# Kernel optimization log

Hardware: AMD Instinct MI355X
Metric: run time of the kernel (lower is better)

Reference implementation:

```python
import jax, jax.numpy as jnp
import numpy as np

WINDOW = 11      # window_size init kwarg
SIGMA = 1.5      # hardcoded in kornia ssim
MAX_VAL = 1.0
EPS = 1e-12
C1 = (0.01 * MAX_VAL) ** 2
C2 = (0.03 * MAX_VAL) ** 2


def _gauss1d():
    # matches kornia get_gaussian_kernel1d for odd window
    x = jnp.arange(WINDOW, dtype=jnp.float32) - WINDOW // 2
    g = jnp.exp(-(x ** 2) / (2.0 * SIGMA ** 2))
    return g / jnp.sum(g)


def _gfilter(x, g):
    # separable depthwise gaussian filter with reflect padding (kornia filter2d default)
    B, C, H, W = x.shape
    p = WINDOW // 2
    xp = jnp.pad(x, ((0, 0), (0, 0), (p, p), (p, p)), mode='reflect')
    kv = jnp.broadcast_to(g.reshape(1, 1, WINDOW, 1), (C, 1, WINDOW, 1))
    kh = jnp.broadcast_to(g.reshape(1, 1, 1, WINDOW), (C, 1, 1, WINDOW))
    dn = ('NCHW', 'OIHW', 'NCHW')
    y = jax.lax.conv_general_dilated(xp, kv, (1, 1), 'VALID',
                                     dimension_numbers=dn, feature_group_count=C)
    y = jax.lax.conv_general_dilated(y, kh, (1, 1), 'VALID',
                                     dimension_numbers=dn, feature_group_count=C)
    return y


def setup_inputs() -> dict:
    key = jax.random.key(0)
    k1, k2 = jax.random.split(key)
    shape = (16, 3, 512, 512)
    img1 = jax.random.uniform(k1, shape, dtype=jnp.float32)
    img2 = jax.random.uniform(k2, shape, dtype=jnp.float32)
    return {"img1": img1, "img2": img2}


def reference(img1, img2):
    g = _gauss1d()
    mu1 = _gfilter(img1, g)
    mu2 = _gfilter(img2, g)
    mu1_sq = mu1 ** 2
    mu2_sq = mu2 ** 2
    mu1_mu2 = mu1 * mu2
    sigma1_sq = _gfilter(img1 ** 2, g) - mu1_sq
    sigma2_sq = _gfilter(img2 ** 2, g) - mu2_sq
    sigma12 = _gfilter(img1 * img2, g) - mu1_mu2
    num = (2.0 * mu1_mu2 + C1) * (2.0 * sigma12 + C2)
    den = (mu1_sq + mu2_sq + C1) * (sigma1_sq + sigma2_sq + C2)
    return num / (den + EPS)
```

## Files before the change

### kernel.cpp

```cpp
#include <hip/hip_runtime.h>
#include <stdint.h>

#define IW 512
#define IH 512
#define NPLANES 48
#define TX 128
#define TY 16
#define INR (TY + 10)
#define BUFW 144
#define SLOTS 8

typedef float f32x2 __attribute__((ext_vector_type(2)));

typedef __attribute__((address_space(1))) const uint32_t guint_t;
typedef __attribute__((address_space(3))) uint32_t luint_t;

#define WAITVM_(n) asm volatile("s_waitcnt vmcnt(" #n ")" ::: "memory")
#define WAITVM(n) WAITVM_(n)

static __device__ __forceinline__ f32x2 pk_mul(f32x2 a, f32x2 b) {
    f32x2 d; asm("v_pk_mul_f32 %0, %1, %2" : "=v"(d) : "v"(a), "v"(b)); return d;
}
static __device__ __forceinline__ f32x2 pk_fma_s(f32x2 a, f32x2 w, f32x2 c) {
    f32x2 d; asm("v_pk_fma_f32 %0, %1, %2, %3" : "=v"(d) : "v"(a), "s"(w), "v"(c)); return d;
}
static __device__ __forceinline__ f32x2 pk_mul_bh(f32x2 a, f32x2 w) {
    f32x2 d; asm("v_pk_mul_f32 %0, %1, %2 op_sel:[1,0] op_sel_hi:[1,1]"
                 : "=v"(d) : "v"(a), "s"(w)); return d;
}
static __device__ __forceinline__ f32x2 pk_fma_bh(f32x2 a, f32x2 w, f32x2 c) {
    f32x2 d; asm("v_pk_fma_f32 %0, %1, %2, %3 op_sel:[1,0,0] op_sel_hi:[1,1,1]"
                 : "=v"(d) : "v"(a), "s"(w), "v"(c)); return d;
}
static __device__ __forceinline__ f32x2 pk_fma_bl(f32x2 a, f32x2 w, f32x2 c) {
    f32x2 d; asm("v_pk_fma_f32 %0, %1, %2, %3 op_sel:[0,0,0] op_sel_hi:[0,1,1]"
                 : "=v"(d) : "v"(a), "s"(w), "v"(c)); return d;
}
static __device__ __forceinline__ float rcp_fast(float x) {
    float d; asm("v_rcp_f32 %0, %1" : "=v"(d) : "v"(x)); return d;
}

__device__ __forceinline__ int refl(int c) {
    c = (c < 0) ? -c : c;
    return (c > IW - 1) ? (2 * (IW - 1) - c) : c;
}

#define W0 0.00102838f
#define W1 0.00759873f
#define W2 0.03600078f
#define W3 0.10936070f
#define W4 0.21300555f
#define W5 0.26601174f
#define W6 0.21300555f
#define W7 0.10936070f
#define W8 0.03600078f
#define W9 0.00759873f
#define W10 0.00102838f

#define SSIM_BODY(JJ, HR, ISSUE_D, WAITN)                                       \
  {                                                                             \
    const int hr = (HR);                                                        \
    const int rs = hr & 7;                                                      \
    if (ISSUE_D) {                                                              \
        const int rr = refl(ty + hr);                  \
        const int ws = (hr + 5) & 7;                                            \
        if (dmaok) {                                                            \
            __builtin_amdgcn_global_load_lds((guint_t*)(p1 + (size_t)rr * IW + gcol), \
                                             (luint_t*)&buf[ws][0][0], 16, 0, 0);     \
            __builtin_amdgcn_global_load_lds((guint_t*)(p2 + (size_t)rr * IW + gcol), \
                                             (luint_t*)&buf[ws][1][0], 16, 0, 0);     \
        }                                                                       \
    }                                                                           \
    WAITVM(WAITN);                                                              \
     \
    f32x2 a1[7], a2[7];                                                         \
    {                                                                           \
        const f32x2* bp1 = (const f32x2*)&buf[rs][0][2 * l + 2];                \
        const f32x2* bp2 = (const f32x2*)&buf[rs][1][2 * l + 2];                \
        _Pragma("unroll")                                                       \
        for (int i = 0; i < 7; ++i) { a1[i] = bp1[i]; a2[i] = bp2[i]; }         \
    }                                                                           \
                                  \
    if (tx == 0) {                                                              \
        _Pragma("unroll")                                                       \
        for (int i = 1; i <= 5; ++i) {                                          \
            const int j = 2 * l + 2 + i;                                        \
            if (j < 8) {                                                        \
                const float v1 = buf[rs][0][16 - j];                            \
                const float v2 = buf[rs][1][16 - j];                            \
                if (i & 1) { a1[i >> 1].y = v1; a2[i >> 1].y = v2; }            \
                else       { a1[i >> 1].x = v1; a2[i >> 1].x = v2; }            \
            }                                                                   \
        }                                                                       \
    } else if (tx == IW - TX) {                                                 \
        _Pragma("unroll")                                                       \
        for (int i = 8; i <= 12; ++i) {                                         \
            const int j = 2 * l + 2 + i;                                        \
            if (j >= 136) {                                                     \
                const float v1 = buf[rs][0][270 - j];                           \
                const float v2 = buf[rs][1][270 - j];                           \
                if (i & 1) { a1[i >> 1].y = v1; a2[i >> 1].y = v2; }            \
                else       { a1[i >> 1].x = v1; a2[i >> 1].x = v2; }            \
            }                                                                   \
        }                                                                       \
    }                                                                           \
                               \
    f32x2 H0, H1, H2, H3, H4;                                                   \
    {                              \
        const f32x2 Q11 = pk_mul(a1[0], a1[0]);                                 \
        const f32x2 Q22 = pk_mul(a2[0], a2[0]);                                 \
        const f32x2 Q12 = pk_mul(a1[0], a2[0]);                                 \
        H0 = pk_mul_bh(a1[0], WH[0]);                                           \
        H1 = pk_mul_bh(a2[0], WH[0]);                                           \
        H2 = pk_mul_bh(Q11,  WH[0]);                                            \
        H3 = pk_mul_bh(Q22,  WH[0]);                                            \
        H4 = pk_mul_bh(Q12,  WH[0]);                                            \
    }                                                                           \
    _Pragma("unroll")                                                           \
    for (int i = 1; i <= 5; ++i) {                                              \
        const f32x2 Q11 = pk_mul(a1[i], a1[i]);                                 \
        const f32x2 Q22 = pk_mul(a2[i], a2[i]);                                 \
        const f32x2 Q12 = pk_mul(a1[i], a2[i]);                                 \
        H0 = pk_fma_bl(a1[i], WL[i], H0); H0 = pk_fma_bh(a1[i], WH[i], H0);     \
        H1 = pk_fma_bl(a2[i], WL[i], H1); H1 = pk_fma_bh(a2[i], WH[i], H1);     \
        H2 = pk_fma_bl(Q11,  WL[i], H2); H2 = pk_fma_bh(Q11,  WH[i], H2);       \
        H3 = pk_fma_bl(Q22,  WL[i], H3); H3 = pk_fma_bh(Q22,  WH[i], H3);       \
        H4 = pk_fma_bl(Q12,  WL[i], H4); H4 = pk_fma_bh(Q12,  WH[i], H4);       \
    }                                                                           \
    {                             \
        const f32x2 Q11 = pk_mul(a1[6], a1[6]);                                 \
        const f32x2 Q22 = pk_mul(a2[6], a2[6]);                                 \
        const f32x2 Q12 = pk_mul(a1[6], a2[6]);                                 \
        H0 = pk_fma_bl(a1[6], WL[6], H0);                                       \
        H1 = pk_fma_bl(a2[6], WL[6], H1);                                       \
        H2 = pk_fma_bl(Q11,  WL[6], H2);                                        \
        H3 = pk_fma_bl(Q22,  WL[6], H3);                                        \
        H4 = pk_fma_bl(Q12,  WL[6], H4);                                        \
    }                                                                           \
                                             \
    _Pragma("unroll")                                                           \
    for (int k = 0; k < 11; ++k) {                                              \
        const int o = hr - k;                                      \
        if (o >= 0 && o < TY) {                                                 \
            const int s = (((JJ) - k) % 11 + 11) % 11;        \
            const f32x2 w2 = {gw[k], gw[k]};                                    \
            acc[s][0] = pk_fma_s(H0, w2, acc[s][0]);                            \
            acc[s][1] = pk_fma_s(H1, w2, acc[s][1]);                            \
            acc[s][2] = pk_fma_s(H2, w2, acc[s][2]);                            \
            acc[s][3] = pk_fma_s(H3, w2, acc[s][3]);                            \
            acc[s][4] = pk_fma_s(H4, w2, acc[s][4]);                            \
        }                                                                       \
    }                                                                           \
                          \
    if (hr >= 10) {                                                             \
        const int o = hr - 10;                                                  \
        const int sc = ((JJ) + 1) % 11;                       \
        const f32x2 mu1 = acc[sc][0], mu2 = acc[sc][1];                         \
        const f32x2 m11 = acc[sc][2], m22 = acc[sc][3], m12 = acc[sc][4];       \
        const f32x2 mu1s = mu1 * mu1, mu2s = mu2 * mu2, mu12 = mu1 * mu2;       \
        const f32x2 s1 = m11 - mu1s, s2 = m22 - mu2s, s12 = m12 - mu12;         \
        const f32x2 num = (2.f * mu12 + 1e-4f) * (2.f * s12 + 9e-4f);           \
        f32x2 den = (mu1s + mu2s + 1e-4f) * (s1 + s2 + 9e-4f);                  \
        den = den + 1e-12f;                                                     \
        f32x2 rd; rd.x = rcp_fast(den.x); rd.y = rcp_fast(den.y);               \
        const f32x2 res = num * rd;                                             \
        _Pragma("unroll")                                                       \
        for (int a = 0; a < 5; ++a) { acc[sc][a].x = 0.f; acc[sc][a].y = 0.f; } \
        *(f32x2*)&po[(size_t)(ty + o) * IW + tx + 2 * l] = res;                 \
    }                                                                           \
  }

__launch_bounds__(64, 3)
__global__ void ssim_kernel(const float* __restrict__ img1,
                            const float* __restrict__ img2,
                            float* __restrict__ out)
{
    __shared__ float buf[SLOTS][2][BUFW];

    const int l  = threadIdx.x;
    const int tx = blockIdx.x * TX;
    const int ty = blockIdx.y * TY;
    const size_t pb = (size_t)blockIdx.z * (size_t)(IW * IH);
    const float* p1 = img1 + pb;
    const float* p2 = img2 + pb;
    float* po = out + pb;

    const float gw[11] = {W0,W1,W2,W3,W4,W5,W6,W7,W8,W9,W10};
    const f32x2 WH[6] = { {W0, 0.f}, {W2, W1}, {W4, W3}, {W6, W5}, {W8, W7}, {W10, W9} };
    const f32x2 WL[7] = { {0.f,0.f}, {W1, W0}, {W3, W2}, {W5, W4}, {W7, W6}, {W9, W8}, {0.f, W10} };

    const int gcol = tx - 8 + 4 * l;
    const bool dmaok = (l < 36) && (gcol >= 0) && (gcol < IW);

    #pragma unroll
    for (int pr = 0; pr < 5; ++pr) {
        const int r = refl(ty - 5 + pr);
        if (dmaok) {
            __builtin_amdgcn_global_load_lds((guint_t*)(p1 + (size_t)r * IW + gcol),
                                             (luint_t*)&buf[pr][0][0], 16, 0, 0);
            __builtin_amdgcn_global_load_lds((guint_t*)(p2 + (size_t)r * IW + gcol),
                                             (luint_t*)&buf[pr][1][0], 16, 0, 0);
        }
    }

    f32x2 acc[11][5];
    #pragma unroll
    for (int s = 0; s < 11; ++s) {
        #pragma unroll
        for (int a = 0; a < 5; ++a) { acc[s][a].x = 0.f; acc[s][a].y = 0.f; }
    }

    for (int hrb = 0; hrb < 22; hrb += 11) {
        #pragma unroll
        for (int jj = 0; jj < 11; ++jj) {
            SSIM_BODY(jj, hrb + jj, true, 10)
        }
    }
    SSIM_BODY(0, 22, false, 8)
    SSIM_BODY(1, 23, false, 6)
    SSIM_BODY(2, 24, false, 4)
    SSIM_BODY(3, 25, false, 2)
    WAITVM(0);
}

extern "C" void kernel_launch(void* const* d_in, const int* in_sizes, int n_in,
                              void* d_out, int out_size, void* d_ws, size_t ws_size,
                              hipStream_t stream) {
    const float* img1 = (const float*)d_in[0];
    const float* img2 = (const float*)d_in[1];
    float* out = (float*)d_out;
    dim3 grid(IW / TX, IH / TY, NPLANES);
    ssim_kernel<<<grid, dim3(64), 0, stream>>>(img1, img2, out);
}
```

Before: 81.31 us.

## Double tile height and software-pipeline row loads with horizontal compute

Doubles the rows per block from 16 to 32, so the 10-row vertical halo is amortized over more output rows. The loop is restructured so the LDS window read for the next row is issued after the current row's horizontal pass, overlapping load latency with compute. Launch bounds drop from 3 to 2 waves per unit to allow more registers for the held-ahead window. The trade is fewer blocks, lower occupancy and a deeper wait schedule that must stay correct against the 8-slot LDS ring.

After: 88.61 us. +9.0%, slower.

```diff
diff --git a/kernel.cpp b/kernel.cpp
--- a/kernel.cpp
+++ b/kernel.cpp
@@ -5,7 +5,7 @@
 #define IH 512
 #define NPLANES 48
 #define TX 128
-#define TY 16
+#define TY 32
 #define INR (TY + 10)
 #define BUFW 144
 #define SLOTS 8
@@ -57,54 +57,53 @@
 #define W9 0.00759873f
 #define W10 0.00102838f
 
-#define SSIM_BODY(JJ, HR, ISSUE_D, WAITN)                                       \
-  {                                                                             \
-    const int hr = (HR);                                                        \
-    const int rs = hr & 7;                                                      \
-    if (ISSUE_D) {                                                              \
-        const int rr = refl(ty + hr);                  \
-        const int ws = (hr + 5) & 7;                                            \
+#define ISSUE_ROW(HR5)                                                          \
+    {                                                                           \
+        const int rr = refl(ty - 5 + (HR5));                                    \
+        const int ws = (HR5) & 7;                                               \
         if (dmaok) {                                                            \
             __builtin_amdgcn_global_load_lds((guint_t*)(p1 + (size_t)rr * IW + gcol), \
                                              (luint_t*)&buf[ws][0][0], 16, 0, 0);     \
             __builtin_amdgcn_global_load_lds((guint_t*)(p2 + (size_t)rr * IW + gcol), \
                                              (luint_t*)&buf[ws][1][0], 16, 0, 0);     \
         }                                                                       \
-    }                                                                           \
-    WAITVM(WAITN);                                                              \
-     \
-    f32x2 a1[7], a2[7];                                                         \
+    }
+
+#define READ_WINDOW(RS)                                                         \
     {                                                                           \
-        const f32x2* bp1 = (const f32x2*)&buf[rs][0][2 * l + 2];                \
-        const f32x2* bp2 = (const f32x2*)&buf[rs][1][2 * l + 2];                \
+        const f32x2* bp1 = (const f32x2*)&buf[RS][0][2 * l + 2];                \
+        const f32x2* bp2 = (const f32x2*)&buf[RS][1][2 * l + 2];                \
         _Pragma("unroll")                                                       \
         for (int i = 0; i < 7; ++i) { a1[i] = bp1[i]; a2[i] = bp2[i]; }         \
-    }                                                                           \
-                                  \
-    if (tx == 0) {                                                              \
-        _Pragma("unroll")                                                       \
-        for (int i = 1; i <= 5; ++i) {                                          \
-            const int j = 2 * l + 2 + i;                                        \
-            if (j < 8) {                                                        \
-                const float v1 = buf[rs][0][16 - j];                            \
-                const float v2 = buf[rs][1][16 - j];                            \
-                if (i & 1) { a1[i >> 1].y = v1; a2[i >> 1].y = v2; }            \
-                else       { a1[i >> 1].x = v1; a2[i >> 1].x = v2; }            \
+        if (tx == 0) {                                                          \
+            _Pragma("unroll")                                                   \
+            for (int i = 1; i <= 5; ++i) {                                      \
+                const int j = 2 * l + 2 + i;                                    \
+                if (j < 8) {                                                    \
+                    const float v1 = buf[RS][0][16 - j];                        \
+                    const float v2 = buf[RS][1][16 - j];                        \
+                    if (i & 1) { a1[i >> 1].y = v1; a2[i >> 1].y = v2; }        \
+                    else       { a1[i >> 1].x = v1; a2[i >> 1].x = v2; }        \
+                }                                                               \
+            }                                                                   \
+        } else if (tx == IW - TX) {                                             \
+            _Pragma("unroll")                                                   \
+            for (int i = 8; i <= 12; ++i) {                                     \
+                const int j = 2 * l + 2 + i;                                    \
+                if (j >= 136) {                                                 \
+                    const float v1 = buf[RS][0][270 - j];                       \
+                    const float v2 = buf[RS][1][270 - j];                       \
+                    if (i & 1) { a1[i >> 1].y = v1; a2[i >> 1].y = v2; }        \
+                    else       { a1[i >> 1].x = v1; a2[i >> 1].x = v2; }        \
+                }                                                               \
             }                                                                   \
         }                                                                       \
-    } else if (tx == IW - TX) {                                                 \
-        _Pragma("unroll")                                                       \
-        for (int i = 8; i <= 12; ++i) {                                         \
-            const int j = 2 * l + 2 + i;                                        \
-            if (j >= 136) {                                                     \
-                const float v1 = buf[rs][0][270 - j];                           \
-                const float v2 = buf[rs][1][270 - j];                           \
-                if (i & 1) { a1[i >> 1].y = v1; a2[i >> 1].y = v2; }            \
-                else       { a1[i >> 1].x = v1; a2[i >> 1].x = v2; }            \
-            }                                                                   \
-        }                                                                       \
-    }                                                                           \
-                               \
+    }
+
+#define SSIM_STEP(JJ, HR, DO_ISSUE, WAITN, DO_READ)                             \
+  {                                                                             \
+    const int hr = (HR);                                                        \
+     \
     f32x2 H0, H1, H2, H3, H4;                                                   \
     {                              \
         const f32x2 Q11 = pk_mul(a1[0], a1[0]);                                 \
@@ -137,7 +136,13 @@
         H3 = pk_fma_bl(Q22,  WL[6], H3);                                        \
         H4 = pk_fma_bl(Q12,  WL[6], H4);                                        \
     }                                                                           \
-                                             \
+                   \
+    if (DO_ISSUE) ISSUE_ROW(hr + 5);                                            \
+    if (DO_READ) {                                                              \
+        WAITVM(WAITN);                                                          \
+        READ_WINDOW((hr + 1) & 7);                                              \
+    }                                                                           \
+                                   \
     _Pragma("unroll")                                                           \
     for (int k = 0; k < 11; ++k) {                                              \
         const int o = hr - k;                                      \
@@ -151,7 +156,7 @@
             acc[s][4] = pk_fma_s(H4, w2, acc[s][4]);                            \
         }                                                                       \
     }                                                                           \
-                          \
+                \
     if (hr >= 10) {                                                             \
         const int o = hr - 10;                                                  \
         const int sc = ((JJ) + 1) % 11;                       \
@@ -170,7 +175,7 @@
     }                                                                           \
   }
 
-__launch_bounds__(64, 3)
+__launch_bounds__(64, 2)
 __global__ void ssim_kernel(const float* __restrict__ img1,
                             const float* __restrict__ img2,
                             float* __restrict__ out)
@@ -194,13 +199,7 @@
 
     #pragma unroll
     for (int pr = 0; pr < 5; ++pr) {
-        const int r = refl(ty - 5 + pr);
-        if (dmaok) {
-            __builtin_amdgcn_global_load_lds((guint_t*)(p1 + (size_t)r * IW + gcol),
-                                             (luint_t*)&buf[pr][0][0], 16, 0, 0);
-            __builtin_amdgcn_global_load_lds((guint_t*)(p2 + (size_t)r * IW + gcol),
-                                             (luint_t*)&buf[pr][1][0], 16, 0, 0);
-        }
+        ISSUE_ROW(pr)
     }
 
     f32x2 acc[11][5];
@@ -210,17 +209,25 @@
         for (int a = 0; a < 5; ++a) { acc[s][a].x = 0.f; acc[s][a].y = 0.f; }
     }
 
-    for (int hrb = 0; hrb < 22; hrb += 11) {
+    f32x2 a1[7], a2[7];
+    WAITVM(8);
+    READ_WINDOW(0)
+
+    for (int hrb = 0; hrb < 33; hrb += 11) {
         #pragma unroll
         for (int jj = 0; jj < 11; ++jj) {
-            SSIM_BODY(jj, hrb + jj, true, 10)
+            SSIM_STEP(jj, hrb + jj, 1, 8, 1)
         }
     }
-    SSIM_BODY(0, 22, false, 8)
-    SSIM_BODY(1, 23, false, 6)
-    SSIM_BODY(2, 24, false, 4)
-    SSIM_BODY(3, 25, false, 2)
-    WAITVM(0);
+    SSIM_STEP(0, 33, 1, 8, 1)
+    SSIM_STEP(1, 34, 1, 8, 1)
+    SSIM_STEP(2, 35, 1, 8, 1)
+    SSIM_STEP(3, 36, 1, 8, 1)
+    SSIM_STEP(4, 37, 0, 6, 1)
+    SSIM_STEP(5, 38, 0, 4, 1)
+    SSIM_STEP(6, 39, 0, 2, 1)
+    SSIM_STEP(7, 40, 0, 0, 1)
+    SSIM_STEP(8, 41, 0, 0, 0)
 }
 
 extern "C" void kernel_launch(void* const* d_in, const int* in_sizes, int n_in,
```

## Swap filter order: vertical pass in registers, horizontal pass via LDS per output row

Applied to the files above, without the earlier changes.

Each block now covers a full 512-wide image row strip of 32 rows with 256 threads. Every thread loads two columns straight from global memory with a two-row register prefetch, in place of the async global-to-LDS DMA ring. The vertical Gaussian pass accumulates the raw moments in registers. Each finished row of the five moments is written to a double-buffered LDS row and filtered horizontally after a barrier. This cuts the horizontal halo overhead and horizontal FMA work per input row, but adds a block-wide barrier per output row and drops the async load pipelining.

Result: slower. 93.50 us (+15.0%).

```diff
diff --git a/kernel.cpp b/kernel.cpp
--- a/kernel.cpp
+++ b/kernel.cpp
@@ -4,19 +4,11 @@
 #define IW 512
 #define IH 512
 #define NPLANES 48
-#define TX 128
-#define TY 16
+#define TY 32
 #define INR (TY + 10)
-#define BUFW 144
-#define SLOTS 8
+#define VB_W 528
 
 typedef float f32x2 __attribute__((ext_vector_type(2)));
-
-typedef __attribute__((address_space(1))) const uint32_t guint_t;
-typedef __attribute__((address_space(3))) uint32_t luint_t;
-
-#define WAITVM_(n) asm volatile("s_waitcnt vmcnt(" #n ")" ::: "memory")
-#define WAITVM(n) WAITVM_(n)
 
 static __device__ __forceinline__ f32x2 pk_mul(f32x2 a, f32x2 b) {
     f32x2 d; asm("v_pk_mul_f32 %0, %1, %2" : "=v"(d) : "v"(a), "v"(b)); return d;
@@ -40,9 +32,9 @@
     float d; asm("v_rcp_f32 %0, %1" : "=v"(d) : "v"(x)); return d;
 }
 
-__device__ __forceinline__ int refl(int c) {
-    c = (c < 0) ? -c : c;
-    return (c > IW - 1) ? (2 * (IW - 1) - c) : c;
+__device__ __forceinline__ int reflr(int r) {
+    r = (r < 0) ? -r : r;
+    return (r > IH - 1) ? (2 * (IH - 1) - r) : r;
 }
 
 #define W0 0.00102838f
@@ -57,106 +49,92 @@
 #define W9 0.00759873f
 #define W10 0.00102838f
 
-#define SSIM_BODY(JJ, HR, ISSUE_D, WAITN)                                       \
+#define SSIM_BODY(B)                                                            \
   {                                                                             \
-    const int hr = (HR);                                                        \
-    const int rs = hr & 7;                                                      \
-    if (ISSUE_D) {                                                              \
-        const int rr = refl(ty + hr);                  \
-        const int ws = (hr + 5) & 7;                                            \
-        if (dmaok) {                                                            \
-            __builtin_amdgcn_global_load_lds((guint_t*)(p1 + (size_t)rr * IW + gcol), \
-                                             (luint_t*)&buf[ws][0][0], 16, 0, 0);     \
-            __builtin_amdgcn_global_load_lds((guint_t*)(p2 + (size_t)rr * IW + gcol), \
-                                             (luint_t*)&buf[ws][1][0], 16, 0, 0);     \
-        }                                                                       \
-    }                                                                           \
-    WAITVM(WAITN);                                                              \
-     \
-    f32x2 a1[7], a2[7];                                                         \
-    {                                                                           \
-        const f32x2* bp1 = (const f32x2*)&buf[rs][0][2 * l + 2];                \
-        const f32x2* bp2 = (const f32x2*)&buf[rs][1][2 * l + 2];                \
-        _Pragma("unroll")                                                       \
-        for (int i = 0; i < 7; ++i) { a1[i] = bp1[i]; a2[i] = bp2[i]; }         \
-    }                                                                           \
-                                  \
-    if (tx == 0) {                                                              \
-        _Pragma("unroll")                                                       \
-        for (int i = 1; i <= 5; ++i) {                                          \
-            const int j = 2 * l + 2 + i;                                        \
-            if (j < 8) {                                                        \
-                const float v1 = buf[rs][0][16 - j];                            \
-                const float v2 = buf[rs][1][16 - j];                            \
-                if (i & 1) { a1[i >> 1].y = v1; a2[i >> 1].y = v2; }            \
-                else       { a1[i >> 1].x = v1; a2[i >> 1].x = v2; }            \
-            }                                                                   \
-        }                                                                       \
-    } else if (tx == IW - TX) {                                                 \
-        _Pragma("unroll")                                                       \
-        for (int i = 8; i <= 12; ++i) {                                         \
-            const int j = 2 * l + 2 + i;                                        \
-            if (j >= 136) {                                                     \
-                const float v1 = buf[rs][0][270 - j];                           \
-                const float v2 = buf[rs][1][270 - j];                           \
-                if (i & 1) { a1[i >> 1].y = v1; a2[i >> 1].y = v2; }            \
-                else       { a1[i >> 1].x = v1; a2[i >> 1].x = v2; }            \
-            }                                                                   \
-        }                                                                       \
-    }                                                                           \
-                               \
-    f32x2 H0, H1, H2, H3, H4;                                                   \
-    {                              \
-        const f32x2 Q11 = pk_mul(a1[0], a1[0]);                                 \
-        const f32x2 Q22 = pk_mul(a2[0], a2[0]);                                 \
-        const f32x2 Q12 = pk_mul(a1[0], a2[0]);                                 \
-        H0 = pk_mul_bh(a1[0], WH[0]);                                           \
-        H1 = pk_mul_bh(a2[0], WH[0]);                                           \
-        H2 = pk_mul_bh(Q11,  WH[0]);                                            \
-        H3 = pk_mul_bh(Q22,  WH[0]);                                            \
-        H4 = pk_mul_bh(Q12,  WH[0]);                                            \
-    }                                                                           \
-    _Pragma("unroll")                                                           \
-    for (int i = 1; i <= 5; ++i) {                                              \
-        const f32x2 Q11 = pk_mul(a1[i], a1[i]);                                 \
-        const f32x2 Q22 = pk_mul(a2[i], a2[i]);                                 \
-        const f32x2 Q12 = pk_mul(a1[i], a2[i]);                                 \
-        H0 = pk_fma_bl(a1[i], WL[i], H0); H0 = pk_fma_bh(a1[i], WH[i], H0);     \
-        H1 = pk_fma_bl(a2[i], WL[i], H1); H1 = pk_fma_bh(a2[i], WH[i], H1);     \
-        H2 = pk_fma_bl(Q11,  WL[i], H2); H2 = pk_fma_bh(Q11,  WH[i], H2);       \
-        H3 = pk_fma_bl(Q22,  WL[i], H3); H3 = pk_fma_bh(Q22,  WH[i], H3);       \
-        H4 = pk_fma_bl(Q12,  WL[i], H4); H4 = pk_fma_bh(Q12,  WH[i], H4);       \
-    }                                                                           \
-    {                             \
-        const f32x2 Q11 = pk_mul(a1[6], a1[6]);                                 \
-        const f32x2 Q22 = pk_mul(a2[6], a2[6]);                                 \
-        const f32x2 Q12 = pk_mul(a1[6], a2[6]);                                 \
-        H0 = pk_fma_bl(a1[6], WL[6], H0);                                       \
-        H1 = pk_fma_bl(a2[6], WL[6], H1);                                       \
-        H2 = pk_fma_bl(Q11,  WL[6], H2);                                        \
-        H3 = pk_fma_bl(Q22,  WL[6], H3);                                        \
-        H4 = pk_fma_bl(Q12,  WL[6], H4);                                        \
-    }                                                                           \
-                                             \
-    _Pragma("unroll")                                                           \
-    for (int k = 0; k < 11; ++k) {                                              \
+    const int hr = hrb + (B);                                                   \
+    if (hr < INR) {                                                             \
+                         \
+      f32x2 cur1, cur2;                                                         \
+      if ((B) & 1) { cur1 = rb1; cur2 = rb2; } else { cur1 = ra1; cur2 = ra2; } \
+                                \
+      {                                                                         \
+        const int rr = reflr(ty - 3 + hr);                 \
+        const f32x2 t1 = *(const f32x2*)(c1p + (size_t)rr * IW);                \
+        const f32x2 t2 = *(const f32x2*)(c2p + (size_t)rr * IW);                \
+        if ((B) & 1) { rb1 = t1; rb2 = t2; } else { ra1 = t1; ra2 = t2; }       \
+      }                                                                         \
+                                                 \
+      const f32x2 P11 = pk_mul(cur1, cur1);                                     \
+      const f32x2 P22 = pk_mul(cur2, cur2);                                     \
+      const f32x2 P12 = pk_mul(cur1, cur2);                                     \
+                  \
+      _Pragma("unroll")                                                         \
+      for (int k = 0; k < 11; ++k) {                                            \
         const int o = hr - k;                                      \
         if (o >= 0 && o < TY) {                                                 \
-            const int s = (((JJ) - k) % 11 + 11) % 11;        \
-            const f32x2 w2 = {gw[k], gw[k]};                                    \
-            acc[s][0] = pk_fma_s(H0, w2, acc[s][0]);                            \
-            acc[s][1] = pk_fma_s(H1, w2, acc[s][1]);                            \
-            acc[s][2] = pk_fma_s(H2, w2, acc[s][2]);                            \
-            acc[s][3] = pk_fma_s(H3, w2, acc[s][3]);                            \
-            acc[s][4] = pk_fma_s(H4, w2, acc[s][4]);                            \
+          const int s = ((((B) % 11) - k) % 11 + 11) % 11;    \
+          const f32x2 w2 = {gw[k], gw[k]};                                      \
+          acc[s][0] = pk_fma_s(cur1, w2, acc[s][0]);                            \
+          acc[s][1] = pk_fma_s(cur2, w2, acc[s][1]);                            \
+          acc[s][2] = pk_fma_s(P11,  w2, acc[s][2]);                            \
+          acc[s][3] = pk_fma_s(P22,  w2, acc[s][3]);                            \
+          acc[s][4] = pk_fma_s(P12,  w2, acc[s][4]);                            \
         }                                                                       \
-    }                                                                           \
-                          \
-    if (hr >= 10) {                                                             \
+      }                                                                         \
+            \
+      if (hr >= 10) {                                                           \
         const int o = hr - 10;                                                  \
-        const int sc = ((JJ) + 1) % 11;                       \
-        const f32x2 mu1 = acc[sc][0], mu2 = acc[sc][1];                         \
-        const f32x2 m11 = acc[sc][2], m22 = acc[sc][3], m12 = acc[sc][4];       \
+        const int sc = ((B) % 11 + 1) % 11;                   \
+        float* vb = &vbuf[o & 1][0][0];                                         \
+        _Pragma("unroll")                                                       \
+        for (int a = 0; a < 5; ++a)                                             \
+          *(f32x2*)(vb + a * VB_W + 8 + 2 * T) = acc[sc][a];                    \
+        _Pragma("unroll")                                                       \
+        for (int a = 0; a < 5; ++a) { acc[sc][a].x = 0.f; acc[sc][a].y = 0.f; } \
+             \
+        asm volatile("s_waitcnt lgkmcnt(0)" ::: "memory");                      \
+        __builtin_amdgcn_s_barrier();                                           \
+        asm volatile("" ::: "memory");                                          \
+        f32x2 H[5];                                                             \
+        _Pragma("unroll")                                                       \
+        for (int a = 0; a < 5; ++a) {                                           \
+          const float* base = vb + a * VB_W + 8;        \
+          f32x2 av[7];                    \
+          _Pragma("unroll")                                                     \
+          for (int i = 0; i < 7; ++i)                                           \
+            av[i] = *(const f32x2*)(base + 2 * T - 6 + 2 * i);                  \
+                   \
+          if (T < 3) {                                                          \
+            _Pragma("unroll")                                                   \
+            for (int ii = 1; ii <= 5; ++ii) {                                   \
+              const int j = 2 * T - 6 + ii;                                     \
+              if (j < 0) {                                                      \
+                const float v = base[-j];                                       \
+                if (ii & 1) av[ii >> 1].y = v; else av[ii >> 1].x = v;          \
+              }                                                                 \
+            }                                                                   \
+          } else if (T > 252) {                                                 \
+            _Pragma("unroll")                                                   \
+            for (int ii = 8; ii <= 12; ++ii) {                                  \
+              const int j = 2 * T - 6 + ii;                                     \
+              if (j > 511) {                                                    \
+                const float v = base[1022 - j];                                 \
+                if (ii & 1) av[ii >> 1].y = v; else av[ii >> 1].x = v;          \
+              }                                                                 \
+            }                                                                   \
+          }                                                                     \
+             \
+          f32x2 h = pk_mul_bh(av[0], WH[0]);                                    \
+          _Pragma("unroll")                                                     \
+          for (int i = 1; i <= 5; ++i) {                                        \
+            h = pk_fma_bl(av[i], WL[i], h);                                     \
+            h = pk_fma_bh(av[i], WH[i], h);                                     \
+          }                                                                     \
+          h = pk_fma_bl(av[6], WL[6], h);                                       \
+          H[a] = h;                                                             \
+        }                                                                       \
+        const f32x2 mu1 = H[0], mu2 = H[1];                                     \
+        const f32x2 m11 = H[2], m22 = H[3], m12 = H[4];                         \
         const f32x2 mu1s = mu1 * mu1, mu2s = mu2 * mu2, mu12 = mu1 * mu2;       \
         const f32x2 s1 = m11 - mu1s, s2 = m22 - mu2s, s12 = m12 - mu12;         \
         const f32x2 num = (2.f * mu12 + 1e-4f) * (2.f * s12 + 9e-4f);           \
@@ -164,44 +142,31 @@
         den = den + 1e-12f;                                                     \
         f32x2 rd; rd.x = rcp_fast(den.x); rd.y = rcp_fast(den.y);               \
         const f32x2 res = num * rd;                                             \
-        _Pragma("unroll")                                                       \
-        for (int a = 0; a < 5; ++a) { acc[sc][a].x = 0.f; acc[sc][a].y = 0.f; } \
-        *(f32x2*)&po[(size_t)(ty + o) * IW + tx + 2 * l] = res;                 \
+        *(f32x2*)&po[(size_t)(ty + o) * IW + 2 * T] = res;                      \
+      }                                                                         \
     }                                                                           \
   }
 
-__launch_bounds__(64, 3)
+__launch_bounds__(256, 2)
 __global__ void ssim_kernel(const float* __restrict__ img1,
                             const float* __restrict__ img2,
                             float* __restrict__ out)
 {
-    __shared__ float buf[SLOTS][2][BUFW];
-
-    const int l  = threadIdx.x;
-    const int tx = blockIdx.x * TX;
-    const int ty = blockIdx.y * TY;
-    const size_t pb = (size_t)blockIdx.z * (size_t)(IW * IH);
+    __shared__ float vbuf[2][5][VB_W];
+
+    const int T  = threadIdx.x;
+    const int ty = blockIdx.x * TY;
+    const size_t pb = (size_t)blockIdx.y * (size_t)(IW * IH);
     const float* p1 = img1 + pb;
     const float* p2 = img2 + pb;
     float* po = out + pb;
 
+    const float* c1p = p1 + 2 * T;
+    const float* c2p = p2 + 2 * T;
+
     const float gw[11] = {W0,W1,W2,W3,W4,W5,W6,W7,W8,W9,W10};
     const f32x2 WH[6] = { {W0, 0.f}, {W2, W1}, {W4, W3}, {W6, W5}, {W8, W7}, {W10, W9} };
     const f32x2 WL[7] = { {0.f,0.f}, {W1, W0}, {W3, W2}, {W5, W4}, {W7, W6}, {W9, W8}, {0.f, W10} };
-
-    const int gcol = tx - 8 + 4 * l;
-    const bool dmaok = (l < 36) && (gcol >= 0) && (gcol < IW);
-
-    #pragma unroll
-    for (int pr = 0; pr < 5; ++pr) {
-        const int r = refl(ty - 5 + pr);
-        if (dmaok) {
-            __builtin_amdgcn_global_load_lds((guint_t*)(p1 + (size_t)r * IW + gcol),
-                                             (luint_t*)&buf[pr][0][0], 16, 0, 0);
-            __builtin_amdgcn_global_load_lds((guint_t*)(p2 + (size_t)r * IW + gcol),
-                                             (luint_t*)&buf[pr][1][0], 16, 0, 0);
-        }
-    }
 
     f32x2 acc[11][5];
     #pragma unroll
@@ -210,17 +175,41 @@
         for (int a = 0; a < 5; ++a) { acc[s][a].x = 0.f; acc[s][a].y = 0.f; }
     }
 
-    for (int hrb = 0; hrb < 22; hrb += 11) {
-        #pragma unroll
-        for (int jj = 0; jj < 11; ++jj) {
-            SSIM_BODY(jj, hrb + jj, true, 10)
-        }
+    f32x2 ra1, ra2, rb1, rb2;
+    {
+        const int r0 = reflr(ty - 5);
+        ra1 = *(const f32x2*)(c1p + (size_t)r0 * IW);
+        ra2 = *(const f32x2*)(c2p + (size_t)r0 * IW);
+        const int r1 = reflr(ty - 4);
+        rb1 = *(const f32x2*)(c1p + (size_t)r1 * IW);
+        rb2 = *(const f32x2*)(c2p + (size_t)r1 * IW);
     }
-    SSIM_BODY(0, 22, false, 8)
-    SSIM_BODY(1, 23, false, 6)
-    SSIM_BODY(2, 24, false, 4)
-    SSIM_BODY(3, 25, false, 2)
-    WAITVM(0);
+
+    #pragma unroll 1
+    for (int hrb = 0; hrb < 44; hrb += 22) {
+        SSIM_BODY(0)
+        SSIM_BODY(1)
+        SSIM_BODY(2)
+        SSIM_BODY(3)
+        SSIM_BODY(4)
+        SSIM_BODY(5)
+        SSIM_BODY(6)
+        SSIM_BODY(7)
+        SSIM_BODY(8)
+        SSIM_BODY(9)
+        SSIM_BODY(10)
+        SSIM_BODY(11)
+        SSIM_BODY(12)
+        SSIM_BODY(13)
+        SSIM_BODY(14)
+        SSIM_BODY(15)
+        SSIM_BODY(16)
+        SSIM_BODY(17)
+        SSIM_BODY(18)
+        SSIM_BODY(19)
+        SSIM_BODY(20)
+        SSIM_BODY(21)
+    }
 }
 
 extern "C" void kernel_launch(void* const* d_in, const int* in_sizes, int n_in,
@@ -229,6 +218,6 @@
     const float* img1 = (const float*)d_in[0];
     const float* img2 = (const float*)d_in[1];
     float* out = (float*)d_out;
-    dim3 grid(IW / TX, IH / TY, NPLANES);
-    ssim_kernel<<<grid, dim3(64), 0, stream>>>(img1, img2, out);
-}
+    dim3 grid(IH / TY, NPLANES);
+    ssim_kernel<<<grid, dim3(256), 0, stream>>>(img1, img2, out);
+}
```
